# Optimization experiments

Hardware: AMD Instinct MI355X
Metric: run time of the kernel (lower is better)

## Reference

```python
import jax, jax.numpy as jnp
import numpy as np

B, WIN, NN, F_IN, H = 8, 12, 2000, 8, 64
N = B * WIN * NN          # total graph nodes = 192000
E = 2_000_000             # edges
EPS = 1e-5                # BatchNorm eps
FC1_IN = 2 * H + WIN * F_IN + 1  # 225


def setup_inputs() -> dict:
    key = jax.random.key(0)
    ks = jax.random.split(key, 24)
    s = lambda k, shp: (jax.random.normal(k, shp, jnp.float32) * 0.05)
    d = {}
    d["adj_indices"] = jax.random.randint(ks[0], (2, E), 0, N)
    d["adj_weight"] = jax.random.uniform(ks[1], (E,), jnp.float32)
    d["x"] = jax.random.normal(ks[2], (N, F_IN), jnp.float32)
    d["inner_out"] = jax.random.normal(ks[3], (B * NN,), jnp.float32)
    # GCN layers
    d["W1"] = s(ks[4], (F_IN, H)); d["b1"] = jnp.zeros((H,), jnp.float32)
    d["W2"] = s(ks[5], (H, H));    d["b2"] = jnp.zeros((H,), jnp.float32)
    # BatchNorm affine params
    d["g1"] = jnp.ones((H,), jnp.float32);  d["be1"] = jnp.zeros((H,), jnp.float32)
    d["g2"] = jnp.ones((H,), jnp.float32);  d["be2"] = jnp.zeros((H,), jnp.float32)
    # LSTM 1 (input 2H) and LSTM 2 (input H); torch gate order i,f,g,o
    d["Wih1"] = s(ks[6], (4 * H, 2 * H)); d["Whh1"] = s(ks[7], (4 * H, H))
    d["bih1"] = jnp.zeros((4 * H,), jnp.float32); d["bhh1"] = jnp.zeros((4 * H,), jnp.float32)
    d["Wih2"] = s(ks[8], (4 * H, H)); d["Whh2"] = s(ks[9], (4 * H, H))
    d["bih2"] = jnp.zeros((4 * H,), jnp.float32); d["bhh2"] = jnp.zeros((4 * H,), jnp.float32)
    # FC head
    d["fc1_w"] = s(ks[10], (FC1_IN, H)); d["fc1_b"] = jnp.zeros((H,), jnp.float32)
    d["fc3_w"] = s(ks[11], (H, 1));      d["fc3_b"] = jnp.zeros((1,), jnp.float32)
    return d


def gcn(x, W, b, row, col, w):
    # PyG GCNConv: add self loops (weight 1), symmetric deg^-1/2 normalization,
    # aggregate messages from row (source) into col (target).
    loop = jnp.arange(N)
    r = jnp.concatenate([row, loop])
    c = jnp.concatenate([col, loop])
    ww = jnp.concatenate([w, jnp.ones((N,), w.dtype)])
    deg = jax.ops.segment_sum(ww, c, num_segments=N)
    dis = jnp.where(deg > 0, 1.0 / jnp.sqrt(deg), 0.0)
    norm = dis[r] * ww * dis[c]                      # [E+N]
    h = x @ W                                        # [N,H]
    out = jax.ops.segment_sum(h[r] * norm[:, None], c, num_segments=N)
    return out + b


def bn(x, g, b):  # training-mode BatchNorm1d (batch stats, biased var)
    m = x.mean(0)
    v = x.var(0)
    return (x - m) / jnp.sqrt(v + EPS) * g + b


def lstm(xs, Wih, Whh, bih, bhh):
    # xs: [T, Bn, D]; returns (all hidden states [T,Bn,H], last hidden [Bn,H])
    Bn = xs.shape[1]
    h0 = jnp.zeros((Bn, H), xs.dtype)
    def step(carry, xt):
        h, c = carry
        gates = xt @ Wih.T + h @ Whh.T + bih + bhh
        i, f, g, o = jnp.split(gates, 4, axis=-1)
        c = jax.nn.sigmoid(f) * c + jax.nn.sigmoid(i) * jnp.tanh(g)
        h = jax.nn.sigmoid(o) * jnp.tanh(c)
        return (h, c), h
    (hT, _), ys = jax.lax.scan(step, (h0, h0), xs)
    return ys, hT


def reference(adj_indices, adj_weight, x, inner_out,
              W1, b1, W2, b2, g1, be1, g2, be2,
              Wih1, Whh1, bih1, bhh1, Wih2, Whh2, bih2, bhh2,
              fc1_w, fc1_b, fc3_w, fc3_b):
    row, col = adj_indices[0], adj_indices[1]
    skip = x.reshape(B, WIN, NN, F_IN).transpose(0, 2, 1, 3).reshape(B * NN, WIN * F_IN)
    h1 = bn(jax.nn.relu(gcn(x, W1, b1, row, col, adj_weight)), g1, be1)   # dropout = identity (eval)
    h2 = bn(jax.nn.relu(gcn(h1, W2, b2, row, col, adj_weight)), g2, be2)
    h = jnp.concatenate([h1, h2], axis=1)                                  # [N, 2H]
    seq = h.reshape(B, WIN, NN, 2 * H).transpose(1, 0, 2, 3).reshape(WIN, B * NN, 2 * H)
    y1, hn1 = lstm(seq, Wih1, Whh1, bih1, bhh1)
    _, hn2 = lstm(y1, Wih2, Whh2, bih2, bhh2)
    z = jnp.concatenate([hn1, hn2, inner_out[:, None], skip], axis=1)      # [B*NN, FC1_IN]
    z = jax.nn.relu(z @ fc1_w + fc1_b)
    z = jax.nn.relu(z @ fc3_w + fc3_b)
    return z.reshape(-1)                                                   # [B*NN]
```

## Files before the change

### kernel.cpp

```cpp
#include <hip/hip_runtime.h>
#include <math.h>

#define N_NODES 192000
#define EDGES   2000000
#define HID     64
#define BN_ROWS 16000
#define T_WIN   12
#define B_SZ    8
#define NN_SZ   2000
#define FIN     8
#define BN_EPS  1e-5f

#define NBKT    750
#define NBLKA   1024
#define ACHUNK  1956
#define BKT_CAP 5120

typedef _Float16 f16x2 __attribute__((ext_vector_type(2)));
typedef _Float16 half4 __attribute__((ext_vector_type(4)));
typedef _Float16 half8 __attribute__((ext_vector_type(8)));
typedef float    f32x4 __attribute__((ext_vector_type(4)));
union F16x2U { float f; f16x2 h; };

__device__ __forceinline__ float frcp(float x){
#if __has_builtin(__builtin_amdgcn_rcpf)
    return __builtin_amdgcn_rcpf(x);
#else
    return 1.0f/x;
#endif
}
__device__ __forceinline__ float fsig(float x){ return frcp(1.0f + __expf(-x)); }
__device__ __forceinline__ float ftanh(float x){ return fmaf(2.0f, fsig(2.0f*x), -1.0f); }

__device__ __forceinline__ float packf16(float a, float b){
    F16x2U u; u.h[0] = (_Float16)a; u.h[1] = (_Float16)b; return u.f;
}

__global__ __launch_bounds__(256) void hist_coarse(
        const int* __restrict__ col, unsigned* __restrict__ gcount,
        int* __restrict__ blockbase){
    __shared__ unsigned bh[NBKT];
    int bl = blockIdx.x, tid = threadIdx.x;
    for (int i = tid; i < NBKT; i += 256) bh[i] = 0u;
    __syncthreads();
    int e0 = bl*ACHUNK;
    int e1 = e0 + ACHUNK; if (e1 > EDGES) e1 = EDGES;
    for (int e = e0 + tid*4; e < e1; e += 1024){
        int4 c4 = *(const int4*)&col[e];
        atomicAdd(&bh[((unsigned)c4.x) >> 8], 1u);
        atomicAdd(&bh[((unsigned)c4.y) >> 8], 1u);
        atomicAdd(&bh[((unsigned)c4.z) >> 8], 1u);
        atomicAdd(&bh[((unsigned)c4.w) >> 8], 1u);
    }
    __syncthreads();
    for (int i = tid; i < NBKT; i += 256)
        blockbase[bl*NBKT + i] = (int)atomicAdd(&gcount[i], bh[i]);
}

__global__ __launch_bounds__(1024) void scan_bkt(
        const unsigned* __restrict__ gcount, int* __restrict__ gbase,
        int* __restrict__ offsets){
    __shared__ int sm[1024];
    int tid = threadIdx.x;
    int v = (tid < NBKT) ? (int)gcount[tid] : 0;
    sm[tid] = v;
    __syncthreads();
    #pragma unroll
    for (int off = 1; off < 1024; off <<= 1){
        int t = (tid >= off) ? sm[tid - off] : 0;
        __syncthreads();
        sm[tid] += t;
        __syncthreads();
    }
    if (tid < NBKT) gbase[tid] = sm[tid] - v;
    if (tid == NBKT) gbase[NBKT] = EDGES;
    if (tid == NBKT+1) offsets[N_NODES] = EDGES;
}

__global__ __launch_bounds__(256) void scatter_bucket(
        const int* __restrict__ row, const int* __restrict__ col,
        const float* __restrict__ w, const int* __restrict__ blockbase,
        const int* __restrict__ gbase, int2* __restrict__ rec){
    __shared__ unsigned cur[NBKT];
    int bl = blockIdx.x, tid = threadIdx.x;
    for (int i = tid; i < NBKT; i += 256)
        cur[i] = (unsigned)(gbase[i] + blockbase[bl*NBKT + i]);
    __syncthreads();
    int e0 = bl*ACHUNK;
    int e1 = e0 + ACHUNK; if (e1 > EDGES) e1 = EDGES;
    for (int e = e0 + tid*4; e < e1; e += 1024){
        int4 r4 = *(const int4*)&row[e];
        int4 c4 = *(const int4*)&col[e];
        float4 w4 = *(const float4*)&w[e];
        int cc[4] = {c4.x, c4.y, c4.z, c4.w};
        int rr[4] = {r4.x, r4.y, r4.z, r4.w};
        float wf[4] = {w4.x, w4.y, w4.z, w4.w};
        #pragma unroll
        for (int q = 0; q < 4; q++){
            int c = cc[q];
            unsigned wfix = (unsigned)(wf[q]*16777216.0f + 0.5f);
            if (wfix > 0xFFFFFFu) wfix = 0xFFFFFFu;
            unsigned p = atomicAdd(&cur[((unsigned)c) >> 8], 1u);
            int2 rv; rv.x = rr[q];
            rv.y = (int)((((unsigned)(c & 255)) << 24) | wfix);
            rec[p] = rv;
        }
    }
}

__global__ __launch_bounds__(256) void bucket_csr(
        const int2* __restrict__ rec, const int* __restrict__ gbase,
        int2* __restrict__ edge_s, int* __restrict__ offsets,
        float* __restrict__ dis){
    __shared__ int2 S[BKT_CAP];
    __shared__ unsigned cnt[256];
    __shared__ unsigned wsum[256];
    __shared__ unsigned cur[256];
    __shared__ float dloc[256];
    int b = blockIdx.x, tid = threadIdx.x;
    int k0 = gbase[b], k1 = gbase[b+1];
    int n = k1 - k0;
    cnt[tid] = 0u; wsum[tid] = 0u;
    __syncthreads();
    bool staged = (n <= BKT_CAP);
    for (int i = tid; i < n; i += 256){
        int2 r = rec[k0 + i];
        if (staged) S[i] = r;
        unsigned clow = ((unsigned)r.y) >> 24;
        atomicAdd(&cnt[clow], 1u);
        atomicAdd(&wsum[clow], ((unsigned)r.y) & 0xFFFFFFu);
    }
    __syncthreads();
    unsigned v = cnt[tid];
    float deg = (float)wsum[tid] * (1.0f/16777216.0f);
    float dv = rsqrtf(deg + 1.0f);
    dloc[tid] = dv;
    dis[(b<<8) + tid] = dv;
    #pragma unroll
    for (int off = 1; off < 256; off <<= 1){
        unsigned t = (tid >= off) ? cnt[tid - off] : 0u;
        __syncthreads();
        cnt[tid] += t;
        __syncthreads();
    }
    unsigned excl = cnt[tid] - v;
    cur[tid] = excl;
    offsets[(b<<8) + tid] = k0 + (int)excl;
    __syncthreads();
    for (int i = tid; i < n; i += 256){
        int2 r = staged ? S[i] : rec[k0 + i];
        unsigned clow = ((unsigned)r.y) >> 24;
        unsigned wfix = ((unsigned)r.y) & 0xFFFFFFu;
        float sv = (float)wfix * (1.0f/16777216.0f) * dloc[clow];
        unsigned p = atomicAdd(&cur[clow], 1u);
        int2 o; o.x = r.x; o.y = __float_as_int(sv);
        edge_s[k0 + (int)p] = o;
    }
}

__global__ __launch_bounds__(256) void aggx_k(
        const int* __restrict__ offsets, const int2* __restrict__ edge_s,
        const float* __restrict__ dis, const float* __restrict__ x,
        float* __restrict__ ax){
    int g   = blockIdx.x*32 + (threadIdx.x >> 3);
    int sub = threadIdx.x & 7;
    float d = dis[g];
    float acc = x[(size_t)g*8 + sub]*d*d;
    int k  = offsets[g];
    int k1 = offsets[g+1];
    for (; k+4 <= k1; k += 4){
        int2 e0 = edge_s[k], e1 = edge_s[k+1], e2 = edge_s[k+2], e3 = edge_s[k+3];
        float d0 = dis[e0.x], d1 = dis[e1.x], d2 = dis[e2.x], d3 = dis[e3.x];
        float v0 = x[(size_t)e0.x*8 + sub];
        float v1 = x[(size_t)e1.x*8 + sub];
        float v2 = x[(size_t)e2.x*8 + sub];
        float v3 = x[(size_t)e3.x*8 + sub];
        acc += v0*(d0*__int_as_float(e0.y));
        acc += v1*(d1*__int_as_float(e1.y));
        acc += v2*(d2*__int_as_float(e2.y));
        acc += v3*(d3*__int_as_float(e3.y));
    }
    for (; k < k1; k++){
        int2 e0 = edge_s[k];
        acc += x[(size_t)e0.x*8 + sub]*(dis[e0.x]*__int_as_float(e0.y));
    }
    ax[(size_t)g*8 + sub] = acc;
}

__global__ __launch_bounds__(256) void lin1b_stats(
        const float* __restrict__ ax, const float* __restrict__ W1,
        const float* __restrict__ b1, float* __restrict__ out,
        float* __restrict__ gsum, float* __restrict__ gsq){
    __shared__ float Ws[512];
    for (int i = threadIdx.x; i < 512; i += 256) Ws[i] = W1[i];
    __syncthreads();
    int f = threadIdx.x & 63;
    float wc[8];
    #pragma unroll
    for (int q = 0; q < 8; q++) wc[q] = Ws[q*64 + f];
    float bb = b1[f];
    float s = 0.f, s2 = 0.f;
    int stride = gridDim.x*blockDim.x;
    for (int idx = blockIdx.x*blockDim.x + threadIdx.x; idx < N_NODES*64; idx += stride){
        int j = idx >> 6;
        const float* ar = ax + (size_t)j*8;
        float acc = bb;
        #pragma unroll
        for (int q = 0; q < 8; q++) acc += ar[q]*wc[q];
        float v = fmaxf(acc, 0.f);
        out[idx] = v;
        s += v; s2 += v*v;
    }
    __shared__ float s1m[256], s2m[256];
    s1m[threadIdx.x] = s; s2m[threadIdx.x] = s2;
    __syncthreads();
    if (threadIdx.x < 64){
        float t1 = s1m[threadIdx.x]+s1m[threadIdx.x+64]+s1m[threadIdx.x+128]+s1m[threadIdx.x+192];
        float t2 = s2m[threadIdx.x]+s2m[threadIdx.x+64]+s2m[threadIdx.x+128]+s2m[threadIdx.x+192];
        atomicAdd(&gsum[threadIdx.x], t1);
        atomicAdd(&gsq[threadIdx.x], t2);
    }
}

#define L2ROWS 128
#define XS2    132
__global__ __launch_bounds__(128) void lin2_bn(
        const float* __restrict__ gcnA, const float* __restrict__ gsum,
        const float* __restrict__ gsq, const float* __restrict__ g1,
        const float* __restrict__ be1, const float* __restrict__ W2,
        _Float16* __restrict__ h1H, float* __restrict__ hlinH){
    __shared__ float Ws[64*64];
    __shared__ float xsT[64*XS2];
    int tid = threadIdx.x;
    int r0 = blockIdx.x * L2ROWS;

    for (int i = tid; i < 1024; i += 128)
        *(float4*)&Ws[i*4] = *(const float4*)&W2[i*4];

    int k4 = tid & 15;
    int rb = tid >> 4;
    float scv[4], shv[4];
    #pragma unroll
    for (int q = 0; q < 4; q++){
        int f = k4*4 + q;
        float mean = gsum[f]*(1.0f/(float)N_NODES);
        float var  = fmaxf(gsq[f]*(1.0f/(float)N_NODES) - mean*mean, 0.f);
        float sc_  = g1[f]*rsqrtf(var + BN_EPS);
        scv[q] = sc_; shv[q] = be1[f] - mean*sc_;
    }
    for (int it = 0; it < 16; it++){
        int r = it*8 + rb;
        float4 v = *(const float4*)&gcnA[(size_t)(r0+r)*64 + k4*4];
        v.x = v.x*scv[0]+shv[0]; v.y = v.y*scv[1]+shv[1];
        v.z = v.z*scv[2]+shv[2]; v.w = v.w*scv[3]+shv[3];
        half4 hh;
        hh[0]=(_Float16)v.x; hh[1]=(_Float16)v.y; hh[2]=(_Float16)v.z; hh[3]=(_Float16)v.w;
        *(half4*)&h1H[(size_t)(r0+r)*64 + k4*4] = hh;
        xsT[(k4*4+0)*XS2 + r] = v.x;
        xsT[(k4*4+1)*XS2 + r] = v.y;
        xsT[(k4*4+2)*XS2 + r] = v.z;
        xsT[(k4*4+3)*XS2 + r] = v.w;
    }
    __syncthreads();

    int cg = tid & 7;
    int rg = tid >> 3;
    float acc[8][8];
    #pragma unroll
    for (int i = 0; i < 8; i++)
        #pragma unroll
        for (int j = 0; j < 8; j++) acc[i][j] = 0.f;

    float4 a0 = *(float4*)&xsT[0*XS2 + rg*8];
    float4 a1 = *(float4*)&xsT[0*XS2 + rg*8 + 4];
    float4 w0 = *(float4*)&Ws[0*64 + cg*8];
    float4 w1 = *(float4*)&Ws[0*64 + cg*8 + 4];
    for (int k = 0; k < 64; k++){
        float4 na0, na1, nw0, nw1;
        if (k < 63){
            na0 = *(float4*)&xsT[(k+1)*XS2 + rg*8];
            na1 = *(float4*)&xsT[(k+1)*XS2 + rg*8 + 4];
            nw0 = *(float4*)&Ws[(k+1)*64 + cg*8];
            nw1 = *(float4*)&Ws[(k+1)*64 + cg*8 + 4];
        }
        float ar[8] = {a0.x,a0.y,a0.z,a0.w,a1.x,a1.y,a1.z,a1.w};
        float wcv[8] = {w0.x,w0.y,w0.z,w0.w,w1.x,w1.y,w1.z,w1.w};
        #pragma unroll
        for (int i = 0; i < 8; i++)
            #pragma unroll
            for (int j = 0; j < 8; j++) acc[i][j] += ar[i]*wcv[j];
        a0=na0; a1=na1; w0=nw0; w1=nw1;
    }
    #pragma unroll
    for (int i = 0; i < 8; i++){
        size_t r = (size_t)(r0 + rg*8 + i);
        float4 pk;
        pk.x = packf16(acc[i][0], acc[i][1]);
        pk.y = packf16(acc[i][2], acc[i][3]);
        pk.z = packf16(acc[i][4], acc[i][5]);
        pk.w = packf16(acc[i][6], acc[i][7]);
        *(float4*)&hlinH[r*32 + cg*4] = pk;
    }
}

__global__ __launch_bounds__(256) void gather2h(
        const int* __restrict__ offsets, const int2* __restrict__ edge_s,
        const float* __restrict__ dis, const float* __restrict__ hlinH,
        const float* __restrict__ bias, float* __restrict__ g2Hf){
    int j = blockIdx.x*8 + (threadIdx.x >> 5);
    int p = threadIdx.x & 31;
    float d = dis[j];
    float dd = d*d;
    F16x2U u; u.f = hlinH[(size_t)j*32 + p];
    float ax = (float)u.h[0]*dd;
    float ay = (float)u.h[1]*dd;
    int k  = offsets[j];
    int k1 = offsets[j+1];
    for (; k+4 <= k1; k += 4){
        int2 e0 = edge_s[k], e1 = edge_s[k+1], e2 = edge_s[k+2], e3 = edge_s[k+3];
        float d0 = dis[e0.x], d1 = dis[e1.x], d2 = dis[e2.x], d3 = dis[e3.x];
        F16x2U a, b, c, e;
        a.f = hlinH[(size_t)e0.x*32 + p];
        b.f = hlinH[(size_t)e1.x*32 + p];
        c.f = hlinH[(size_t)e2.x*32 + p];
        e.f = hlinH[(size_t)e3.x*32 + p];
        float n0 = d0*__int_as_float(e0.y), n1 = d1*__int_as_float(e1.y);
        float n2 = d2*__int_as_float(e2.y), n3 = d3*__int_as_float(e3.y);
        ax += (float)a.h[0]*n0; ay += (float)a.h[1]*n0;
        ax += (float)b.h[0]*n1; ay += (float)b.h[1]*n1;
        ax += (float)c.h[0]*n2; ay += (float)c.h[1]*n2;
        ax += (float)e.h[0]*n3; ay += (float)e.h[1]*n3;
    }
    for (; k < k1; k++){
        int2 e0 = edge_s[k];
        F16x2U a; a.f = hlinH[(size_t)e0.x*32 + p];
        float n0 = dis[e0.x]*__int_as_float(e0.y);
        ax += (float)a.h[0]*n0; ay += (float)a.h[1]*n0;
    }
    float2 bv = *(const float2*)&bias[2*p];
    float vx = fmaxf(ax + bv.x, 0.f);
    float vy = fmaxf(ay + bv.y, 0.f);
    F16x2U o; o.h[0] = (_Float16)vx; o.h[1] = (_Float16)vy;
    g2Hf[(size_t)j*32 + p] = o.f;
}

__global__ __launch_bounds__(256) void stats2h(
        const float* __restrict__ g2Hf, float* __restrict__ gsum2, float* __restrict__ gsq2){
    int p = threadIdx.x & 31;
    float s0 = 0.f, s1 = 0.f, q0 = 0.f, q1 = 0.f;
    int stride = gridDim.x*blockDim.x;
    for (int idx = blockIdx.x*blockDim.x + threadIdx.x; idx < N_NODES*32; idx += stride){
        F16x2U u; u.f = g2Hf[idx];
        float vx = (float)u.h[0], vy = (float)u.h[1];
        s0 += vx; q0 += vx*vx;
        s1 += vy; q1 += vy*vy;
    }
    __shared__ float sb[128];
    if (threadIdx.x < 128) sb[threadIdx.x] = 0.f;
    __syncthreads();
    atomicAdd(&sb[2*p],      s0);
    atomicAdd(&sb[2*p+1],    s1);
    atomicAdd(&sb[64+2*p],   q0);
    atomicAdd(&sb[64+2*p+1], q1);
    __syncthreads();
    if (threadIdx.x < 64){
        atomicAdd(&gsum2[threadIdx.x], sb[threadIdx.x]);
        atomicAdd(&gsq2[threadIdx.x],  sb[64+threadIdx.x]);
    }
}

__global__ void prep_weights(const float* __restrict__ Wih1, const float* __restrict__ Whh1,
                             const float* __restrict__ bih1, const float* __restrict__ bhh1,
                             const float* __restrict__ Wih2, const float* __restrict__ Whh2,
                             const float* __restrict__ bih2, const float* __restrict__ bhh2,
                             _Float16* W1F, _Float16* W2F, float* b1c, float* b2c){
    int idx = blockIdx.x*blockDim.x + threadIdx.x;
    if (idx < 6*256*32){
        int kt = idx >> 13;
        int rem = idx & 8191;
        int n = rem >> 5, kin = rem & 31;
        int k = kt*32 + kin;
        float v = (k < 128) ? Wih1[n*128 + k] : Whh1[n*64 + (k-128)];
        W1F[idx] = (_Float16)v;
    }
    int i2 = idx - 6*256*32;
    if (i2 >= 0 && i2 < 4*256*32){
        int kt = i2 >> 13;
        int rem = i2 & 8191;
        int n = rem >> 5, kin = rem & 31;
        int k = kt*32 + kin;
        float v = (k < 64) ? Wih2[n*64 + k] : Whh2[n*64 + (k-64)];
        W2F[i2] = (_Float16)v;
    }
    int i3 = idx - (6*256*32 + 4*256*32);
    if (i3 >= 0 && i3 < 256) b1c[i3] = bih1[i3] + bhh1[i3];
    int i4 = i3 - 256;
    if (i4 >= 0 && i4 < 256) b2c[i4] = bih2[i4] + bhh2[i4];
}

#define X1S 200
#define X2S 136
__global__ __launch_bounds__(256) void lstm_fused(
        const _Float16* __restrict__ h1H, const _Float16* __restrict__ g2H,
        const float* __restrict__ gsum2, const float* __restrict__ gsq2,
        const float* __restrict__ g2bn, const float* __restrict__ be2,
        const _Float16* __restrict__ W1F, const _Float16* __restrict__ W2F,
        const float* __restrict__ b1c, const float* __restrict__ b2c,
        float* __restrict__ h1s, float* __restrict__ h2s){
    __shared__ _Float16 X1h[16*X1S];
    __shared__ _Float16 X2h[16*X2S];
    int tid = threadIdx.x;
    int j0 = blockIdx.x*16;
    int w    = tid >> 6;
    int lane = tid & 63;
    int quad = lane >> 4;
    int l16  = lane & 15;
    int u    = 16*w + l16;

    int c4 = tid & 15;
    int sr = (tid >> 4) & 15;
    int sj = j0 + sr;
    int sb = sj / NN_SZ, sn = sj - sb*NN_SZ;
    size_t rbase = ((size_t)(sb*T_WIN)*NN_SZ + sn)*64 + c4*4;
    float sc2v[4], sh2v[4];
    #pragma unroll
    for (int q = 0; q < 4; q++){
        int f = c4*4 + q;
        float mean = gsum2[f]*(1.0f/(float)N_NODES);
        float var  = fmaxf(gsq2[f]*(1.0f/(float)N_NODES) - mean*mean, 0.f);
        float sc_  = g2bn[f]*rsqrtf(var + BN_EPS);
        sc2v[q] = sc_; sh2v[q] = be2[f] - mean*sc_;
    }

    float c1r[4], c2r[4], h2r[4];
    #pragma unroll
    for (int i = 0; i < 4; i++){ c1r[i] = 0.f; c2r[i] = 0.f; h2r[i] = 0.f; }

    float bi1 = b1c[u], bf1 = b1c[64+u], bg1 = b1c[128+u], bo1 = b1c[192+u];
    float bi2 = b2c[u], bf2 = b2c[64+u], bg2 = b2c[128+u], bo2 = b2c[192+u];

    {
        half4 v0 = *(const half4*)&h1H[rbase];
        half4 g4 = *(const half4*)&g2H[rbase];
        half4 v1;
        #pragma unroll
        for (int q = 0; q < 4; q++) v1[q] = (_Float16)((float)g4[q]*sc2v[q] + sh2v[q]);
        *(half4*)&X1h[sr*X1S + c4*4]       = v0;
        *(half4*)&X1h[sr*X1S + 64 + c4*4]  = v1;
        *(half4*)&X1h[sr*X1S + 128 + c4*4] = (half4){0,0,0,0};
    }
    __syncthreads();

    for (int t = 0; t < T_WIN; t++){
        half4 nv0, ng4;
        if (t < T_WIN-1){
            size_t rb = rbase + (size_t)(t+1)*NN_SZ*64;
            nv0 = *(const half4*)&h1H[rb];
            ng4 = *(const half4*)&g2H[rb];
        }

        f32x4 acc[4];
        #pragma unroll
        for (int g = 0; g < 4; g++) acc[g] = (f32x4){0.f,0.f,0.f,0.f};
        #pragma unroll
        for (int kt = 0; kt < 6; kt++){
            half8 a = *(const half8*)&X1h[l16*X1S + kt*32 + quad*8];
            #pragma unroll
            for (int g = 0; g < 4; g++){
                half8 b = *(const half8*)&W1F[(size_t)(kt*256 + 64*g + u)*32 + quad*8];
                acc[g] = __builtin_amdgcn_mfma_f32_16x16x32_f16(a, b, acc[g], 0, 0, 0);
            }
        }
        __syncthreads();

        #pragma unroll
        for (int r = 0; r < 4; r++){
            int rowl = quad*4 + r;
            float gi = acc[0][r] + bi1;
            float gf = acc[1][r] + bf1;
            float gg = acc[2][r] + bg1;
            float go = acc[3][r] + bo1;
            float cn = fsig(gf)*c1r[r] + fsig(gi)*ftanh(gg);
            float hn = fsig(go)*ftanh(cn);
            c1r[r] = cn;
            X2h[rowl*X2S + u]      = (_Float16)hn;
            X2h[rowl*X2S + 64 + u] = (_Float16)h2r[r];
            X1h[rowl*X1S + 128 + u] = (_Float16)hn;
            if (t == T_WIN-1) h1s[(size_t)(j0 + rowl)*64 + u] = hn;
        }
        if (t < T_WIN-1){
            half4 v1;
            #pragma unroll
            for (int q = 0; q < 4; q++) v1[q] = (_Float16)((float)ng4[q]*sc2v[q] + sh2v[q]);
            *(half4*)&X1h[sr*X1S + c4*4]      = nv0;
            *(half4*)&X1h[sr*X1S + 64 + c4*4] = v1;
        }
        __syncthreads();

        f32x4 acc2[4];
        #pragma unroll
        for (int g = 0; g < 4; g++) acc2[g] = (f32x4){0.f,0.f,0.f,0.f};
        #pragma unroll
        for (int kt = 0; kt < 4; kt++){
            half8 a = *(const half8*)&X2h[l16*X2S + kt*32 + quad*8];
            #pragma unroll
            for (int g = 0; g < 4; g++){
                half8 b = *(const half8*)&W2F[(size_t)(kt*256 + 64*g + u)*32 + quad*8];
                acc2[g] = __builtin_amdgcn_mfma_f32_16x16x32_f16(a, b, acc2[g], 0, 0, 0);
            }
        }

        #pragma unroll
        for (int r = 0; r < 4; r++){
            int rowl = quad*4 + r;
            float gi = acc2[0][r] + bi2;
            float gf = acc2[1][r] + bf2;
            float gg = acc2[2][r] + bg2;
            float go = acc2[3][r] + bo2;
            float cn = fsig(gf)*c2r[r] + fsig(gi)*ftanh(gg);
            float hn = fsig(go)*ftanh(cn);
            c2r[r] = cn;
            h2r[r] = hn;
            if (t == T_WIN-1) h2s[(size_t)(j0 + rowl)*64 + u] = hn;
        }
    }
}

__global__ __launch_bounds__(256) void fc_head(
        const float* __restrict__ h1s, const float* __restrict__ h2s,
        const float* __restrict__ inner, const float* __restrict__ x,
        const float* __restrict__ fc1_w, const float* __restrict__ fc1_b,
        const float* __restrict__ fc3_w, const float* __restrict__ fc3_b,
        float* __restrict__ out){
    __shared__ float zsm[4][226];
    int wv = threadIdx.x >> 6;
    int f  = threadIdx.x & 63;
    int j  = blockIdx.x*4 + wv;
    int b = j / NN_SZ, n = j - b*NN_SZ;
    for (int k = f; k < 225; k += 64){
        float v;
        if (k < 64)        v = h1s[j*64 + k];
        else if (k < 128)  v = h2s[j*64 + (k-64)];
        else if (k == 128) v = inner[j];
        else {
            int kk = k - 129;
            int w_ = kk >> 3, ff = kk & 7;
            v = x[((b*T_WIN + w_)*NN_SZ + n)*FIN + ff];
        }
        zsm[wv][k] = v;
    }
    __syncthreads();
    float acc = fc1_b[f];
    for (int k = 0; k < 225; k++) acc += zsm[wv][k]*fc1_w[k*64 + f];
    float p = fmaxf(acc, 0.f) * fc3_w[f];
    #pragma unroll
    for (int off = 32; off > 0; off >>= 1) p += __shfl_down(p, off, 64);
    if (f == 0) out[j] = fmaxf(p + fc3_b[0], 0.f);
}

extern "C" void kernel_launch(void* const* d_in, const int* in_sizes, int n_in,
                              void* d_out, int out_size, void* d_ws, size_t ws_size,
                              hipStream_t stream){
    const int*   adj  = (const int*)d_in[0];
    const int*   row  = adj;
    const int*   col  = adj + EDGES;
    const float* aw   = (const float*)d_in[1];
    const float* x    = (const float*)d_in[2];
    const float* inner= (const float*)d_in[3];
    const float* W1   = (const float*)d_in[4];
    const float* b1   = (const float*)d_in[5];
    const float* W2   = (const float*)d_in[6];
    const float* b2   = (const float*)d_in[7];
    const float* g1   = (const float*)d_in[8];
    const float* be1  = (const float*)d_in[9];
    const float* g2   = (const float*)d_in[10];
    const float* be2  = (const float*)d_in[11];
    const float* Wih1 = (const float*)d_in[12];
    const float* Whh1 = (const float*)d_in[13];
    const float* bih1 = (const float*)d_in[14];
    const float* bhh1 = (const float*)d_in[15];
    const float* Wih2 = (const float*)d_in[16];
    const float* Whh2 = (const float*)d_in[17];
    const float* bih2 = (const float*)d_in[18];
    const float* bhh2 = (const float*)d_in[19];
    const float* fc1w = (const float*)d_in[20];
    const float* fc1b = (const float*)d_in[21];
    const float* fc3w = (const float*)d_in[22];
    const float* fc3b = (const float*)d_in[23];
    float* out = (float*)d_out;

    float* ws = (float*)d_ws;
    const size_t NB = (size_t)N_NODES*64;
    float* bufX = ws;
    float* bufY = ws + NB;
    float* bufZ = ws + 2*NB;
    int2*  edge_s  = (int2*)(ws + 3*NB);
    float* degdis  = ws + 3*NB + (size_t)2*EDGES;
    float* gsum    = degdis + N_NODES;
    float* gsq     = gsum + 64;
    float* gsum2   = gsq + 64;
    float* gsq2    = gsum2 + 64;
    unsigned* gcount = (unsigned*)(gsq2 + 64);
    int* gbase   = (int*)(gcount + NBKT);
    int* offsets = gbase + (NBKT + 2);

    int* blockbase = (int*)bufX;
    int2* rec      = (int2*)bufY;

    float* hlinH = bufX;
    _Float16* h1H = (_Float16*)bufZ;
    float* ax    = bufZ + (size_t)N_NODES*32 + 64;
    float* gcnA1 = bufY;
    float* g2Hf  = bufY;

    float* h1s = bufX;
    float* h2s = bufX + (size_t)BN_ROWS*64;
    _Float16* W1F = (_Float16*)(bufX + (size_t)4*BN_ROWS*64);
    _Float16* W2F = W1F + 6*256*32;
    float* b1c = (float*)(W2F + 4*256*32);
    float* b2c = b1c + 256;

    hipMemsetAsync(gcount, 0, NBKT*sizeof(unsigned), stream);
    hipMemsetAsync(gsum, 0, 256*sizeof(float), stream);
    hist_coarse   <<<NBLKA, 256, 0, stream>>>(col, gcount, blockbase);
    scan_bkt      <<<1, 1024, 0, stream>>>(gcount, gbase, offsets);
    scatter_bucket<<<NBLKA, 256, 0, stream>>>(row, col, aw, blockbase, gbase, rec);
    bucket_csr    <<<NBKT, 256, 0, stream>>>(rec, gbase, edge_s, offsets, degdis);

    aggx_k<<<N_NODES/32, 256, 0, stream>>>(offsets, edge_s, degdis, x, ax);
    lin1b_stats<<<1024, 256, 0, stream>>>(ax, W1, b1, gcnA1, gsum, gsq);

    lin2_bn<<<N_NODES/L2ROWS, 128, 0, stream>>>(gcnA1, gsum, gsq, g1, be1, W2, h1H, hlinH);

    gather2h<<<N_NODES/8, 256, 0, stream>>>(offsets, edge_s, degdis, hlinH, b2, g2Hf);
    stats2h<<<1024, 256, 0, stream>>>(g2Hf, gsum2, gsq2);

    prep_weights<<<(6*256*32 + 4*256*32 + 512 + 255)/256, 256, 0, stream>>>(
        Wih1, Whh1, bih1, bhh1, Wih2, Whh2, bih2, bhh2, W1F, W2F, b1c, b2c);
    lstm_fused<<<BN_ROWS/16, 256, 0, stream>>>(h1H, (const _Float16*)g2Hf,
                                               gsum2, gsq2, g2, be2,
                                               W1F, W2F, b1c, b2c, h1s, h2s);

    fc_head<<<BN_ROWS/4, 256, 0, stream>>>(h1s, h2s, inner, x, fc1w, fc1b, fc3w, fc3b, out);
}
```

Baseline: 514.7 us.

## Skew LSTM layers across timesteps with double-buffered LDS to halve barriers

Restructures the fused two-layer LSTM loop as a software pipeline. Each iteration now computes layer-2 step t together with layer-1 step t+1, using double-buffered shared-memory tiles, which cuts the barriers per step from two to one and issues both MFMA groups back to back. The MFMA section is wrapped in s_setprio. In exchange it doubles the LDS footprint, adds prologue and epilogue code, and raises register pressure from holding two accumulator sets live.

```diff
diff --git a/kernel.cpp b/kernel.cpp
--- a/kernel.cpp
+++ b/kernel.cpp
@@ -407,8 +407,8 @@
         const _Float16* __restrict__ W1F, const _Float16* __restrict__ W2F,
         const float* __restrict__ b1c, const float* __restrict__ b2c,
         float* __restrict__ h1s, float* __restrict__ h2s){
-    __shared__ _Float16 X1h[16*X1S];
-    __shared__ _Float16 X2h[16*X2S];
+    __shared__ _Float16 X1h[2][16*X1S];
+    __shared__ _Float16 X2h[2][16*X2S];
     int tid = threadIdx.x;
     int j0 = blockIdx.x*16;
     int w    = tid >> 6;
@@ -422,6 +422,7 @@
     int sj = j0 + sr;
     int sb = sj / NN_SZ, sn = sj - sb*NN_SZ;
     size_t rbase = ((size_t)(sb*T_WIN)*NN_SZ + sn)*64 + c4*4;
+    const size_t tstep = (size_t)NN_SZ*64;
     float sc2v[4], sh2v[4];
     #pragma unroll
     for (int q = 0; q < 4; q++){
@@ -445,71 +446,135 @@
         half4 v1;
         #pragma unroll
         for (int q = 0; q < 4; q++) v1[q] = (_Float16)((float)g4[q]*sc2v[q] + sh2v[q]);
-        *(half4*)&X1h[sr*X1S + c4*4]       = v0;
-        *(half4*)&X1h[sr*X1S + 64 + c4*4]  = v1;
-        *(half4*)&X1h[sr*X1S + 128 + c4*4] = (half4){0,0,0,0};
-    }
-    __syncthreads();
-
-    for (int t = 0; t < T_WIN; t++){
-        half4 nv0, ng4;
-        if (t < T_WIN-1){
-            size_t rb = rbase + (size_t)(t+1)*NN_SZ*64;
-            nv0 = *(const half4*)&h1H[rb];
-            ng4 = *(const half4*)&g2H[rb];
-        }
-
-        f32x4 acc[4];
-        #pragma unroll
-        for (int g = 0; g < 4; g++) acc[g] = (f32x4){0.f,0.f,0.f,0.f};
+        *(half4*)&X1h[0][sr*X1S + c4*4]       = v0;
+        *(half4*)&X1h[0][sr*X1S + 64 + c4*4]  = v1;
+        *(half4*)&X1h[0][sr*X1S + 128 + c4*4] = (half4){0,0,0,0};
+    }
+    __syncthreads();
+
+    half4 pv0 = *(const half4*)&h1H[rbase + tstep];
+    half4 pg4 = *(const half4*)&g2H[rbase + tstep];
+
+    {
+        f32x4 acc1[4];
+        #pragma unroll
+        for (int g = 0; g < 4; g++) acc1[g] = (f32x4){0.f,0.f,0.f,0.f};
         #pragma unroll
         for (int kt = 0; kt < 6; kt++){
-            half8 a = *(const half8*)&X1h[l16*X1S + kt*32 + quad*8];
+            half8 a = *(const half8*)&X1h[0][l16*X1S + kt*32 + quad*8];
             #pragma unroll
             for (int g = 0; g < 4; g++){
                 half8 b = *(const half8*)&W1F[(size_t)(kt*256 + 64*g + u)*32 + quad*8];
-                acc[g] = __builtin_amdgcn_mfma_f32_16x16x32_f16(a, b, acc[g], 0, 0, 0);
+                acc1[g] = __builtin_amdgcn_mfma_f32_16x16x32_f16(a, b, acc1[g], 0, 0, 0);
             }
         }
-        __syncthreads();
-
         #pragma unroll
         for (int r = 0; r < 4; r++){
             int rowl = quad*4 + r;
-            float gi = acc[0][r] + bi1;
-            float gf = acc[1][r] + bf1;
-            float gg = acc[2][r] + bg1;
-            float go = acc[3][r] + bo1;
+            float gi = acc1[0][r] + bi1;
+            float gf = acc1[1][r] + bf1;
+            float gg = acc1[2][r] + bg1;
+            float go = acc1[3][r] + bo1;
             float cn = fsig(gf)*c1r[r] + fsig(gi)*ftanh(gg);
             float hn = fsig(go)*ftanh(cn);
             c1r[r] = cn;
-            X2h[rowl*X2S + u]      = (_Float16)hn;
-            X2h[rowl*X2S + 64 + u] = (_Float16)h2r[r];
-            X1h[rowl*X1S + 128 + u] = (_Float16)hn;
-            if (t == T_WIN-1) h1s[(size_t)(j0 + rowl)*64 + u] = hn;
-        }
-        if (t < T_WIN-1){
-            half4 v1;
-            #pragma unroll
-            for (int q = 0; q < 4; q++) v1[q] = (_Float16)((float)ng4[q]*sc2v[q] + sh2v[q]);
-            *(half4*)&X1h[sr*X1S + c4*4]      = nv0;
-            *(half4*)&X1h[sr*X1S + 64 + c4*4] = v1;
-        }
-        __syncthreads();
-
-        f32x4 acc2[4];
-        #pragma unroll
-        for (int g = 0; g < 4; g++) acc2[g] = (f32x4){0.f,0.f,0.f,0.f};
+            X2h[1][rowl*X2S + u]      = (_Float16)hn;
+            X2h[1][rowl*X2S + 64 + u] = (_Float16)0.f;
+            X1h[1][rowl*X1S + 128 + u] = (_Float16)hn;
+        }
+        half4 v1;
+        #pragma unroll
+        for (int q = 0; q < 4; q++) v1[q] = (_Float16)((float)pg4[q]*sc2v[q] + sh2v[q]);
+        *(half4*)&X1h[1][sr*X1S + c4*4]      = pv0;
+        *(half4*)&X1h[1][sr*X1S + 64 + c4*4] = v1;
+    }
+    __syncthreads();
+
+    for (int i = 0; i < T_WIN-1; i++){
+        int rb = (i+1)&1, wb = i&1;
+        half4 nv0, ng4;
+        if (i < T_WIN-2){
+            size_t rbg = rbase + (size_t)(i+2)*tstep;
+            nv0 = *(const half4*)&h1H[rbg];
+            ng4 = *(const half4*)&g2H[rbg];
+        }
+
+        f32x4 acc2[4], acc1[4];
+        #pragma unroll
+        for (int g = 0; g < 4; g++){
+            acc2[g] = (f32x4){0.f,0.f,0.f,0.f};
+            acc1[g] = (f32x4){0.f,0.f,0.f,0.f};
+        }
+        __builtin_amdgcn_s_setprio(1);
         #pragma unroll
         for (int kt = 0; kt < 4; kt++){
-            half8 a = *(const half8*)&X2h[l16*X2S + kt*32 + quad*8];
+            half8 a = *(const half8*)&X2h[rb][l16*X2S + kt*32 + quad*8];
             #pragma unroll
             for (int g = 0; g < 4; g++){
                 half8 b = *(const half8*)&W2F[(size_t)(kt*256 + 64*g + u)*32 + quad*8];
                 acc2[g] = __builtin_amdgcn_mfma_f32_16x16x32_f16(a, b, acc2[g], 0, 0, 0);
             }
         }
-
+        #pragma unroll
+        for (int kt = 0; kt < 6; kt++){
+            half8 a = *(const half8*)&X1h[rb][l16*X1S + kt*32 + quad*8];
+            #pragma unroll
+            for (int g = 0; g < 4; g++){
+                half8 b = *(const half8*)&W1F[(size_t)(kt*256 + 64*g + u)*32 + quad*8];
+                acc1[g] = __builtin_amdgcn_mfma_f32_16x16x32_f16(a, b, acc1[g], 0, 0, 0);
+            }
+        }
+        __builtin_amdgcn_s_setprio(0);
+
+        #pragma unroll
+        for (int r = 0; r < 4; r++){
+            float gi = acc2[0][r] + bi2;
+            float gf = acc2[1][r] + bf2;
+            float gg = acc2[2][r] + bg2;
+            float go = acc2[3][r] + bo2;
+            float cn = fsig(gf)*c2r[r] + fsig(gi)*ftanh(gg);
+            float hn = fsig(go)*ftanh(cn);
+            c2r[r] = cn;
+            h2r[r] = hn;
+        }
+        #pragma unroll
+        for (int r = 0; r < 4; r++){
+            int rowl = quad*4 + r;
+            float gi = acc1[0][r] + bi1;
+            float gf = acc1[1][r] + bf1;
+            float gg = acc1[2][r] + bg1;
+            float go = acc1[3][r] + bo1;
+            float cn = fsig(gf)*c1r[r] + fsig(gi)*ftanh(gg);
+            float hn = fsig(go)*ftanh(cn);
+            c1r[r] = cn;
+            X2h[wb][rowl*X2S + u]      = (_Float16)hn;
+            X2h[wb][rowl*X2S + 64 + u] = (_Float16)h2r[r];
+            if (i < T_WIN-2) X1h[wb][rowl*X1S + 128 + u] = (_Float16)hn;
+            if (i == T_WIN-2) h1s[(size_t)(j0 + rowl)*64 + u] = hn;
+        }
+        if (i < T_WIN-2){
+            half4 v1;
+            #pragma unroll
+            for (int q = 0; q < 4; q++) v1[q] = (_Float16)((float)ng4[q]*sc2v[q] + sh2v[q]);
+            *(half4*)&X1h[wb][sr*X1S + c4*4]      = nv0;
+            *(half4*)&X1h[wb][sr*X1S + 64 + c4*4] = v1;
+        }
+        __syncthreads();
+    }
+
+    {
+        f32x4 acc2[4];
+        #pragma unroll
+        for (int g = 0; g < 4; g++) acc2[g] = (f32x4){0.f,0.f,0.f,0.f};
+        #pragma unroll
+        for (int kt = 0; kt < 4; kt++){
+            half8 a = *(const half8*)&X2h[0][l16*X2S + kt*32 + quad*8];
+            #pragma unroll
+            for (int g = 0; g < 4; g++){
+                half8 b = *(const half8*)&W2F[(size_t)(kt*256 + 64*g + u)*32 + quad*8];
+                acc2[g] = __builtin_amdgcn_mfma_f32_16x16x32_f16(a, b, acc2[g], 0, 0, 0);
+            }
+        }
         #pragma unroll
         for (int r = 0; r < 4; r++){
             int rowl = quad*4 + r;
@@ -519,9 +584,7 @@
             float go = acc2[3][r] + bo2;
             float cn = fsig(gf)*c2r[r] + fsig(gi)*ftanh(gg);
             float hn = fsig(go)*ftanh(cn);
-            c2r[r] = cn;
-            h2r[r] = hn;
-            if (t == T_WIN-1) h2s[(size_t)(j0 + rowl)*64 + u] = hn;
+            h2s[(size_t)(j0 + rowl)*64 + u] = hn;
         }
     }
 }
```

After: 535.4 us. 4.0% more time.
